# Kernel optimization log

Measured on AMD Instinct MI355X. Metric: run time of the kernel, lower is better.

## Reference

```python
import jax, jax.numpy as jnp
import numpy as np

B, S, DIN, DK, DV = 8, 2048, 1024, 1024, 1024


def setup_inputs() -> dict:
    key = jax.random.key(0)
    ks = jax.random.split(key, 9)
    s_in = 1.0 / np.sqrt(DIN)
    return {
        "query": jax.random.normal(ks[0], (B, S, DIN), jnp.float32),
        "key_": jax.random.normal(ks[1], (B, S, DIN), jnp.float32),
        "value": jax.random.normal(ks[2], (B, S, DIN), jnp.float32),
        "Wq_w": jax.random.uniform(ks[3], (DK, DIN), jnp.float32, -s_in, s_in),
        "Wq_b": jax.random.uniform(ks[4], (DK,), jnp.float32, -s_in, s_in),
        "Wk_w": jax.random.uniform(ks[5], (DK, DIN), jnp.float32, -s_in, s_in),
        "Wk_b": jax.random.uniform(ks[6], (DK,), jnp.float32, -s_in, s_in),
        "Wv_w": jax.random.uniform(ks[7], (DV, DIN), jnp.float32, -s_in, s_in),
        "Wv_b": jax.random.uniform(ks[8], (DV,), jnp.float32, -s_in, s_in),
    }


def reference(query, key_, value, Wq_w, Wq_b, Wk_w, Wk_b, Wv_w, Wv_b):
    # Linear projections: x @ W.T + b (torch nn.Linear convention)
    Q = jnp.einsum('bsd,kd->bsk', query, Wq_w) + Wq_b   # [B,S,DK]
    K = jnp.einsum('bsd,kd->bsk', key_, Wk_w) + Wk_b    # [B,S,DK]
    V = jnp.einsum('bsd,vd->bsv', value, Wv_w) + Wv_b   # [B,S,DV]
    scale = 1.0 / jnp.sqrt(jnp.asarray(Q.shape[-1], Q.dtype))
    scores = jnp.einsum('bqk,bsk->bqs', Q, K) * scale   # [B,S,S]
    attn = jax.nn.softmax(scores, axis=-1)
    return jnp.einsum('bqs,bsv->bqv', attn, V)          # [B,S,DV]
```

## Files before the change

kernel.cpp:

```cpp
#include <hip/hip_runtime.h>

typedef unsigned short u16;
typedef float    f32x4  __attribute__((ext_vector_type(4)));
typedef __bf16   bf16x8 __attribute__((ext_vector_type(8)));
typedef u16      u16x4  __attribute__((ext_vector_type(4)));
typedef u16      u16x8  __attribute__((ext_vector_type(8)));

#define NB   8
#define NS   2048
#define ND   1024

__device__ __forceinline__ u16 f2bf(float x) {
    union { float f; unsigned u; } v; v.f = x;
    unsigned r = v.u + 0x7fffu + ((v.u >> 16) & 1u);
    return (u16)(r >> 16);
}
__device__ __forceinline__ float bf2f(u16 x) {
    union { unsigned u; float f; } v; v.u = ((unsigned)x) << 16;
    return v.f;
}

__global__ __launch_bounds__(256) void cvt_f32_bf16(const float* __restrict__ in,
                                                    u16* __restrict__ out, int n4) {
    int i = blockIdx.x * 256 + threadIdx.x;
    if (i >= n4) return;
    f32x4 v = ((const f32x4*)in)[i];
    u16x4 o;
    o[0] = f2bf(v[0]); o[1] = f2bf(v[1]); o[2] = f2bf(v[2]); o[3] = f2bf(v[3]);
    ((u16x4*)out)[i] = o;
}

template<int OUT_BF16, int BIAS>
__global__ __launch_bounds__(512, 2)
void gemm256_kernel(const u16* __restrict__ A, long long sA, int lda,
                    const u16* __restrict__ B, long long sB, int ldb,
                    void* __restrict__ Cv, long long sC, int ldc,
                    const float* __restrict__ bias, int K)
{
    __shared__ alignas(16) u16 lds[49152];

    const int gx = gridDim.x, gy = gridDim.y;
    const int nwg = gx * gy * (int)gridDim.z;
    const int lin = blockIdx.x + gx * (blockIdx.y + gy * blockIdx.z);
    const int chunk = nwg >> 3;
    const int swz = (lin & 7) * chunk + (lin >> 3);
    const int bx = swz % gx;
    const int tq = swz / gx;
    const int by = tq % gy;
    const int bz = tq / gy;

    A += sA * bz;
    B += sB * bz;

    const int row0 = by << 8, col0 = bx << 8;
    const int t = threadIdx.x;
    const int w = t >> 6, l = t & 63;
    const int wm = w >> 2, wn = w & 3;

    const int j0e = ((l & 3) ^ ((l >> 3) & 3)) << 3;
    const u16* gA0 = A + (long long)(row0 + (w << 4) + (l >> 2)) * lda + j0e;
    const u16* gA1 = gA0 + ((long long)lda << 7);
    const u16* gB0 = B + (long long)(col0 + (w << 4) + (l >> 2)) * ldb + j0e;
    const u16* gB1 = gB0 + ((long long)ldb << 7);
    const unsigned dA0 = (unsigned)(w << 10);

    auto STAGE = [&](int buf, int kt) {
        const unsigned bo = (unsigned)buf * 32768u;
        __builtin_amdgcn_global_load_lds((__attribute__((address_space(1))) void*)(gA0 + kt),
            (__attribute__((address_space(3))) void*)((char*)lds + bo + dA0),          16, 0, 0);
        __builtin_amdgcn_global_load_lds((__attribute__((address_space(1))) void*)(gA1 + kt),
            (__attribute__((address_space(3))) void*)((char*)lds + bo + dA0 + 8192),   16, 0, 0);
        __builtin_amdgcn_global_load_lds((__attribute__((address_space(1))) void*)(gB0 + kt),
            (__attribute__((address_space(3))) void*)((char*)lds + bo + 16384 + dA0),  16, 0, 0);
        __builtin_amdgcn_global_load_lds((__attribute__((address_space(1))) void*)(gB1 + kt),
            (__attribute__((address_space(3))) void*)((char*)lds + bo + 16384 + dA0 + 8192), 16, 0, 0);
    };

    const int lr  = l & 15;
    const int jsw = ((l >> 4) ^ ((lr >> 1) & 3)) << 4;
    const int aA  = ((wm << 7) + lr) * 64 + jsw;
    const int aB  = 16384 + ((wn << 6) + lr) * 64 + jsw;

    f32x4 acc[8][4] = {};
    const int NT = K >> 5;

    STAGE(0, 0);
    STAGE(1, 32);

    for (int tt = 0; tt < NT; ++tt) {
        if (tt + 2 < NT) {
            STAGE((tt + 2) % 3, (tt + 2) << 5);
            asm volatile("s_waitcnt vmcnt(8)" ::: "memory");
        } else if (tt + 1 < NT) {
            asm volatile("s_waitcnt vmcnt(4)" ::: "memory");
        } else {
            asm volatile("s_waitcnt vmcnt(0)" ::: "memory");
        }
        __builtin_amdgcn_s_barrier();

        const char* bufp = (const char*)lds + (tt % 3) * 32768;
        bf16x8 af[8], bfv[4];
#pragma unroll
        for (int mf = 0; mf < 8; ++mf) af[mf]  = *(const bf16x8*)(bufp + aA + mf * 1024);
#pragma unroll
        for (int nf = 0; nf < 4; ++nf) bfv[nf] = *(const bf16x8*)(bufp + aB + nf * 1024);

        asm volatile("s_waitcnt lgkmcnt(0)" ::: "memory");
        __builtin_amdgcn_s_barrier();

        __builtin_amdgcn_s_setprio(1);
#pragma unroll
        for (int mf = 0; mf < 8; ++mf)
#pragma unroll
            for (int nf = 0; nf < 4; ++nf)
                acc[mf][nf] = __builtin_amdgcn_mfma_f32_16x16x32_bf16(af[mf], bfv[nf], acc[mf][nf], 0, 0, 0);
        __builtin_amdgcn_s_setprio(0);
    }

    const int fr = l & 15, fq = (l >> 4) << 2;
    u16*   Cb = (u16*)Cv + sC * bz;
    float* Cf = (float*)Cv + sC * bz;
#pragma unroll
    for (int mf = 0; mf < 8; ++mf) {
        const int r = row0 + (wm << 7) + (mf << 4) + fq;
#pragma unroll
        for (int nf = 0; nf < 4; ++nf) {
            const int c = col0 + (wn << 6) + (nf << 4) + fr;
#pragma unroll
            for (int j = 0; j < 4; ++j) {
                float vv = acc[mf][nf][j];
                if (BIAS == 1) vv += bias[c];
                else if (BIAS == 2) vv += bias[r + j];
                if (OUT_BF16) Cb[(long long)(r + j) * ldc + c] = f2bf(vv);
                else          Cf[(long long)(r + j) * ldc + c] = vv;
            }
        }
    }
}

__global__ __launch_bounds__(256, 4)
void softmax_kernel(u16* __restrict__ sc, float scale2) {
    u16* row = sc + (long long)blockIdx.x * NS;
    const int t = threadIdx.x;
    u16x8 a = ((const u16x8*)row)[t];
    float x[8];
#pragma unroll
    for (int j = 0; j < 8; ++j) x[j] = bf2f(a[j]);
    float m = x[0];
#pragma unroll
    for (int j = 1; j < 8; ++j) m = fmaxf(m, x[j]);
#pragma unroll
    for (int off = 1; off < 64; off <<= 1) m = fmaxf(m, __shfl_xor(m, off));
    __shared__ float red[2][4];
    const int w = t >> 6;
    if ((t & 63) == 0) red[0][w] = m;
    __syncthreads();
    m = fmaxf(fmaxf(red[0][0], red[0][1]), fmaxf(red[0][2], red[0][3]));
    float e[8], s = 0.f;
#pragma unroll
    for (int j = 0; j < 8; ++j) { e[j] = exp2f((x[j] - m) * scale2); s += e[j]; }
#pragma unroll
    for (int off = 1; off < 64; off <<= 1) s += __shfl_xor(s, off);
    if ((t & 63) == 0) red[1][w] = s;
    __syncthreads();
    s = red[1][0] + red[1][1] + red[1][2] + red[1][3];
    const float inv = 1.0f / s;
    u16x8 o;
#pragma unroll
    for (int j = 0; j < 8; ++j) o[j] = f2bf(e[j] * inv);
    ((u16x8*)row)[t] = o;
}

extern "C" void kernel_launch(void* const* d_in, const int* in_sizes, int n_in,
                              void* d_out, int out_size, void* d_ws, size_t ws_size,
                              hipStream_t stream) {
    const float* q  = (const float*)d_in[0];
    const float* k  = (const float*)d_in[1];
    const float* v  = (const float*)d_in[2];
    const float* wq = (const float*)d_in[3];
    const float* bq = (const float*)d_in[4];
    const float* wk = (const float*)d_in[5];
    const float* bk = (const float*)d_in[6];
    const float* wv = (const float*)d_in[7];
    const float* bv = (const float*)d_in[8];
    float* out = (float*)d_out;

    char* ws = (char*)d_ws;
    const long long NIN = (long long)NB * NS * ND;
    const long long NW  = (long long)ND * ND;
    const long long NSC = (long long)NB * NS * NS;

    u16* SCB = (u16*)ws;
    u16* X   = (u16*)ws;
    u16* W   = X + NIN;
    u16* QB  = SCB + NSC;
    u16* KB  = QB + NIN;
    u16* VT  = KB + NIN;
    (void)ws_size; (void)in_sizes; (void)n_in; (void)out_size;

    cvt_f32_bf16<<<16384, 256, 0, stream>>>(q,  X, (int)(NIN / 4));
    cvt_f32_bf16<<<1024,  256, 0, stream>>>(wq, W, (int)(NW / 4));
    gemm256_kernel<1, 1><<<dim3(4, 64, 1), 512, 0, stream>>>(
        X, 0, ND, W, 0, ND, QB, 0, ND, bq, ND);

    cvt_f32_bf16<<<16384, 256, 0, stream>>>(k,  X, (int)(NIN / 4));
    cvt_f32_bf16<<<1024,  256, 0, stream>>>(wk, W, (int)(NW / 4));
    gemm256_kernel<1, 1><<<dim3(4, 64, 1), 512, 0, stream>>>(
        X, 0, ND, W, 0, ND, KB, 0, ND, bk, ND);

    cvt_f32_bf16<<<16384, 256, 0, stream>>>(v,  X, (int)(NIN / 4));
    cvt_f32_bf16<<<1024,  256, 0, stream>>>(wv, W, (int)(NW / 4));
    gemm256_kernel<1, 2><<<dim3(8, 4, NB), 512, 0, stream>>>(
        W, 0, ND, X, (long long)NS * ND, ND, VT, (long long)ND * NS, NS, bv, ND);

    gemm256_kernel<1, 0><<<dim3(8, 8, NB), 512, 0, stream>>>(
        QB, (long long)NS * ND, ND, KB, (long long)NS * ND, ND,
        SCB, (long long)NS * NS, NS, nullptr, ND);

    const float scale2 = (1.0f / 32.0f) * 1.44269504088896f;
    softmax_kernel<<<NB * NS, 256, 0, stream>>>(SCB, scale2);

    gemm256_kernel<0, 0><<<dim3(4, 8, NB), 512, 0, stream>>>(
        SCB, (long long)NS * NS, NS,
        VT, (long long)ND * NS, NS,
        out, (long long)NS * ND, ND, nullptr, NS);
}
```

Baseline: 506.8 us.

## Restructure GEMM main loop into 64-wide K tiles with quadrant-interleaved loads and MFMAs

```diff
diff --git a/kernel.cpp b/kernel.cpp
--- a/kernel.cpp
+++ b/kernel.cpp
@@ -30,6 +30,11 @@
     ((u16x4*)out)[i] = o;
 }
 
+#define GLL(src, dst) __builtin_amdgcn_global_load_lds( \
+    (const __attribute__((address_space(1))) void*)(src), \
+    (__attribute__((address_space(3))) void*)((char*)lds + (dst)), 16, 0, 0)
+#define MFMA16(a, b, c) __builtin_amdgcn_mfma_f32_16x16x32_bf16(a, b, c, 0, 0, 0)
+
 template<int OUT_BF16, int BIAS>
 __global__ __launch_bounds__(512, 2)
 void gemm256_kernel(const u16* __restrict__ A, long long sA, int lda,
@@ -37,7 +42,7 @@
                     void* __restrict__ Cv, long long sC, int ldc,
                     const float* __restrict__ bias, int K)
 {
-    __shared__ alignas(16) u16 lds[49152];
+    __shared__ alignas(16) u16 lds[65536];
 
     const int gx = gridDim.x, gy = gridDim.y;
     const int nwg = gx * gy * (int)gridDim.z;
@@ -56,64 +61,118 @@
     const int t = threadIdx.x;
     const int w = t >> 6, l = t & 63;
     const int wm = w >> 2, wn = w & 3;
-
-    const int j0e = ((l & 3) ^ ((l >> 3) & 3)) << 3;
-    const u16* gA0 = A + (long long)(row0 + (w << 4) + (l >> 2)) * lda + j0e;
-    const u16* gA1 = gA0 + ((long long)lda << 7);
-    const u16* gB0 = B + (long long)(col0 + (w << 4) + (l >> 2)) * ldb + j0e;
-    const u16* gB1 = gB0 + ((long long)ldb << 7);
-    const unsigned dA0 = (unsigned)(w << 10);
-
-    auto STAGE = [&](int buf, int kt) {
-        const unsigned bo = (unsigned)buf * 32768u;
-        __builtin_amdgcn_global_load_lds((__attribute__((address_space(1))) void*)(gA0 + kt),
-            (__attribute__((address_space(3))) void*)((char*)lds + bo + dA0),          16, 0, 0);
-        __builtin_amdgcn_global_load_lds((__attribute__((address_space(1))) void*)(gA1 + kt),
-            (__attribute__((address_space(3))) void*)((char*)lds + bo + dA0 + 8192),   16, 0, 0);
-        __builtin_amdgcn_global_load_lds((__attribute__((address_space(1))) void*)(gB0 + kt),
-            (__attribute__((address_space(3))) void*)((char*)lds + bo + 16384 + dA0),  16, 0, 0);
-        __builtin_amdgcn_global_load_lds((__attribute__((address_space(1))) void*)(gB1 + kt),
-            (__attribute__((address_space(3))) void*)((char*)lds + bo + 16384 + dA0 + 8192), 16, 0, 0);
+    const int lr = l & 15, hi = l >> 4;
+
+    const int tr = t >> 3, ts = t & 7;
+    const int scol = ((ts ^ (tr & 7)) << 3);
+    const u16* gA = A + (long long)(row0 + tr) * lda + scol;
+    const u16* gB = B + (long long)(col0 + tr) * ldb + scol;
+    const unsigned sdst = (unsigned)(t << 4);
+
+    auto STAGE_A = [&](unsigned bufb, int kt, int h) {
+        const u16* g = gA + (long long)(h << 7) * lda + kt;
+        const unsigned d = bufb + (unsigned)(h << 14) + sdst;
+        GLL(g, d);
+        GLL(g + ((long long)lda << 6), d + 8192u);
     };
-
-    const int lr  = l & 15;
-    const int jsw = ((l >> 4) ^ ((lr >> 1) & 3)) << 4;
-    const int aA  = ((wm << 7) + lr) * 64 + jsw;
-    const int aB  = 16384 + ((wn << 6) + lr) * 64 + jsw;
+    auto STAGE_B = [&](unsigned bufb, int kt, int h) {
+        const u16* g = gB + (long long)(h << 7) * ldb + kt;
+        const unsigned d = bufb + 32768u + (unsigned)(h << 14) + sdst;
+        GLL(g, d);
+        GLL(g + ((long long)ldb << 6), d + 8192u);
+    };
+
+    const unsigned sw0    = (unsigned)((hi ^ (lr & 7)) << 4);
+    const unsigned aAbase = (unsigned)(wm * 16384 + lr * 128);
+    const unsigned aBbase = 32768u + (unsigned)((wn >> 1) * 16384 + ((wn & 1) * 64 + lr) * 128);
 
     f32x4 acc[8][4] = {};
-    const int NT = K >> 5;
-
-    STAGE(0, 0);
-    STAGE(1, 32);
+    bf16x8 av[4][2], bv[4][2];
+    const int NT = K >> 6;
+
+    STAGE_A(0, 0, 0); STAGE_A(0, 0, 1); STAGE_B(0, 0, 0); STAGE_B(0, 0, 1);
 
     for (int tt = 0; tt < NT; ++tt) {
-        if (tt + 2 < NT) {
-            STAGE((tt + 2) % 3, (tt + 2) << 5);
-            asm volatile("s_waitcnt vmcnt(8)" ::: "memory");
-        } else if (tt + 1 < NT) {
-            asm volatile("s_waitcnt vmcnt(4)" ::: "memory");
-        } else {
-            asm volatile("s_waitcnt vmcnt(0)" ::: "memory");
-        }
-        __builtin_amdgcn_s_barrier();
-
-        const char* bufp = (const char*)lds + (tt % 3) * 32768;
-        bf16x8 af[8], bfv[4];
-#pragma unroll
-        for (int mf = 0; mf < 8; ++mf) af[mf]  = *(const bf16x8*)(bufp + aA + mf * 1024);
-#pragma unroll
-        for (int nf = 0; nf < 4; ++nf) bfv[nf] = *(const bf16x8*)(bufp + aB + nf * 1024);
-
+        const unsigned cb = (unsigned)((tt & 1) << 16);
+        const unsigned nb = (unsigned)((~tt & 1) << 16);
+        const int kt1 = (tt + 1) << 6;
+        const bool st = (tt + 1 < NT);
+
+        asm volatile("s_waitcnt vmcnt(0)" ::: "memory");
+        __builtin_amdgcn_s_barrier();
+
+#pragma unroll
+        for (int m = 0; m < 4; ++m) {
+            av[m][0] = *(const bf16x8*)((const char*)lds + cb + aAbase + m * 2048 + sw0);
+            av[m][1] = *(const bf16x8*)((const char*)lds + cb + aAbase + m * 2048 + (sw0 ^ 64u));
+        }
+#pragma unroll
+        for (int n = 0; n < 2; ++n) {
+            bv[n][0] = *(const bf16x8*)((const char*)lds + cb + aBbase + n * 2048 + sw0);
+            bv[n][1] = *(const bf16x8*)((const char*)lds + cb + aBbase + n * 2048 + (sw0 ^ 64u));
+        }
+        if (st) { STAGE_A(nb, kt1, 0); STAGE_A(nb, kt1, 1); }
+        __builtin_amdgcn_s_barrier();
         asm volatile("s_waitcnt lgkmcnt(0)" ::: "memory");
-        __builtin_amdgcn_s_barrier();
-
-        __builtin_amdgcn_s_setprio(1);
-#pragma unroll
-        for (int mf = 0; mf < 8; ++mf)
-#pragma unroll
-            for (int nf = 0; nf < 4; ++nf)
-                acc[mf][nf] = __builtin_amdgcn_mfma_f32_16x16x32_bf16(af[mf], bfv[nf], acc[mf][nf], 0, 0, 0);
+        __builtin_amdgcn_sched_barrier(0);
+        __builtin_amdgcn_s_setprio(1);
+#pragma unroll
+        for (int m = 0; m < 4; ++m)
+#pragma unroll
+            for (int n = 0; n < 2; ++n) {
+                acc[m][n] = MFMA16(av[m][0], bv[n][0], acc[m][n]);
+                acc[m][n] = MFMA16(av[m][1], bv[n][1], acc[m][n]);
+            }
+        __builtin_amdgcn_s_setprio(0);
+        __builtin_amdgcn_s_barrier();
+
+#pragma unroll
+        for (int n = 2; n < 4; ++n) {
+            bv[n][0] = *(const bf16x8*)((const char*)lds + cb + aBbase + n * 2048 + sw0);
+            bv[n][1] = *(const bf16x8*)((const char*)lds + cb + aBbase + n * 2048 + (sw0 ^ 64u));
+        }
+        if (st) { STAGE_B(nb, kt1, 0); STAGE_B(nb, kt1, 1); }
+        __builtin_amdgcn_s_barrier();
+        asm volatile("s_waitcnt lgkmcnt(0)" ::: "memory");
+        __builtin_amdgcn_sched_barrier(0);
+        __builtin_amdgcn_s_setprio(1);
+#pragma unroll
+        for (int m = 0; m < 4; ++m)
+#pragma unroll
+            for (int n = 2; n < 4; ++n) {
+                acc[m][n] = MFMA16(av[m][0], bv[n][0], acc[m][n]);
+                acc[m][n] = MFMA16(av[m][1], bv[n][1], acc[m][n]);
+            }
+        __builtin_amdgcn_s_setprio(0);
+        __builtin_amdgcn_s_barrier();
+
+#pragma unroll
+        for (int m = 0; m < 4; ++m) {
+            av[m][0] = *(const bf16x8*)((const char*)lds + cb + aAbase + (m + 4) * 2048 + sw0);
+            av[m][1] = *(const bf16x8*)((const char*)lds + cb + aAbase + (m + 4) * 2048 + (sw0 ^ 64u));
+        }
+        __builtin_amdgcn_s_barrier();
+        asm volatile("s_waitcnt lgkmcnt(0)" ::: "memory");
+        __builtin_amdgcn_sched_barrier(0);
+        __builtin_amdgcn_s_setprio(1);
+#pragma unroll
+        for (int m = 0; m < 4; ++m)
+#pragma unroll
+            for (int n = 0; n < 2; ++n) {
+                acc[m + 4][n] = MFMA16(av[m][0], bv[n][0], acc[m + 4][n]);
+                acc[m + 4][n] = MFMA16(av[m][1], bv[n][1], acc[m + 4][n]);
+            }
+        __builtin_amdgcn_s_setprio(0);
+        __builtin_amdgcn_s_barrier();
+
+        __builtin_amdgcn_s_setprio(1);
+#pragma unroll
+        for (int m = 0; m < 4; ++m)
+#pragma unroll
+            for (int n = 2; n < 4; ++n) {
+                acc[m + 4][n] = MFMA16(av[m][0], bv[n][0], acc[m + 4][n]);
+                acc[m + 4][n] = MFMA16(av[m][1], bv[n][1], acc[m + 4][n]);
+            }
         __builtin_amdgcn_s_setprio(0);
     }
 
```

Result: faster. 493.2 us (-2.7%).
